# Kernel tuning notes

Measured on AMD Instinct MI355X. Metric: run time of the kernel, lower is better.

The kernel has to match this reference:

```python
import jax, jax.numpy as jnp
import numpy as np

CONF_THRES = 0.4
IOU_THRES = 0.45
MAX_WH = 4096.0   # class offset for non-agnostic NMS (torch code: max_wh)
K_PRE = 1024      # candidates kept for the O(K^2) NMS stage (<= max_nms=30000)
MAX_DET = 300     # max detections per image (torch default)
B, N, NC = 16, 25200, 80


def xywh2xyxy(x):
    xy, wh = x[..., :2], x[..., 2:4]
    return jnp.concatenate([xy - wh * 0.5, xy + wh * 0.5], axis=-1)


def box_iou(a, b):
    # a: [K,4], b: [K,4] in xyxy
    area_a = (a[:, 2] - a[:, 0]) * (a[:, 3] - a[:, 1])
    area_b = (b[:, 2] - b[:, 0]) * (b[:, 3] - b[:, 1])
    lt = jnp.maximum(a[:, None, :2], b[None, :, :2])
    rb = jnp.minimum(a[:, None, 2:], b[None, :, 2:])
    inter = jnp.clip(rb - lt, 0.0, None).prod(-1)
    return inter / (area_a[:, None] + area_b[None, :] - inter + 1e-7)


def _nms_single(pred, conf_logit, logit, head):
    # pred [N,85] (decoded, sigmoided), conf_logit [N,5] raw, logit [N,80] raw, head [N]
    xc = pred[:, 4] > CONF_THRES                      # objectness gate
    obj_sig = jax.nn.sigmoid(conf_logit[:, 4:5])      # [N,1]
    log_sig = jax.nn.sigmoid(logit) * obj_sig         # sel_prob == 'objclass'
    cls_scores = pred[:, 5:] * pred[:, 4:5]           # x[:,5:] *= x[:,4:5]
    box = xywh2xyxy(pred[:, :4])                      # [N,4]
    conf = cls_scores.max(axis=1)                     # best class conf
    j = cls_scores.argmax(axis=1).astype(pred.dtype)  # best class id
    valid = xc & (conf > CONF_THRES)
    score = jnp.where(valid, conf, 0.0)
    # top-K candidates (sorted descending) -> fixed-shape NMS
    top_s, top_i = jax.lax.top_k(score, K_PRE)
    valid_k = top_s > 0.0
    boxes_k = box[top_i] + j[top_i, None] * MAX_WH    # per-class box offset (agnostic=False)
    iou = box_iou(boxes_k, boxes_k)                   # [K,K]
    idx = jnp.arange(K_PRE)

    def body(i, keep):
        sup = (iou[i] > IOU_THRES) & (idx > i) & keep[i]
        return keep & ~sup

    keep = jax.lax.fori_loop(0, K_PRE, body, valid_k)
    final_score = jnp.where(keep, top_s, 0.0)
    _, sel = jax.lax.top_k(final_score, MAX_DET)      # first MAX_DET survivors
    gi = top_i[sel]
    m = (final_score[sel] > 0.0).astype(pred.dtype)[:, None]  # validity mask
    det = jnp.concatenate([box[gi], conf[gi, None], j[gi, None]], axis=1)  # [300,6] xyxy,conf,cls
    # pack: det(6) | class logits*obj(80) | obj_conf(1) | classHead(1) | valid(1) -> [300,89]
    return jnp.concatenate(
        [det * m, log_sig[gi] * m, obj_sig[gi] * m, head[gi, None] * m, m], axis=1)


def setup_inputs() -> dict:
    key = jax.random.key(0)
    k1, k2, k3, k4, k5, k6 = jax.random.split(key, 6)
    xy = jax.random.uniform(k1, (B, N, 2), jnp.float32) * 640.0
    wh = 2.0 + jax.random.uniform(k2, (B, N, 2), jnp.float32) * 198.0
    objcls = jax.random.uniform(k3, (B, N, 1 + NC), jnp.float32)
    prediction = jnp.concatenate([xy, wh, objcls], axis=-1)       # [B,N,85]
    pred_conf_logits = jax.random.normal(k4, (B, N, 5), jnp.float32)
    logits = jax.random.normal(k5, (B, N, NC), jnp.float32)
    class_head = jax.random.randint(k6, (B, N), 0, 3).astype(jnp.float32)
    return {"prediction": prediction, "pred_conf_logits": pred_conf_logits,
            "logits": logits, "class_head": class_head}


def reference(prediction, pred_conf_logits, logits, class_head):
    return jax.vmap(_nms_single)(prediction, pred_conf_logits, logits, class_head)
```

## Files before the change

### kernel.cpp

```cpp
#include <hip/hip_runtime.h>
#include <math.h>

#define BATCH 16
#define NN 25200
#define NCLS 80
#define K_PRE 1024
#define MAX_DET 300
#define CONF_T 0.4f
#define IOU_T 0.45f
#define TBIAS 0x3E000000u
#define RROWS 128
#define STHREADS 512

__global__ void __launch_bounds__(STHREADS) score_kernel(
    const float* __restrict__ pred, unsigned long long* __restrict__ keys) {
    __shared__ float srow[RROWS * 85];

    const int tile = blockIdx.x, b = blockIdx.y, tid = threadIdx.x;
    const int row0 = tile * RROWS;
    int nrows = NN - row0;
    if (nrows > RROWS) nrows = RROWS;

    const float4* g4 = (const float4*)(pred + ((size_t)b * NN + row0) * 85);
    float4* l4 = (float4*)srow;
    const int nf4 = (nrows * 85) >> 2;
    for (int i = tid; i < nf4; i += STHREADS) l4[i] = g4[i];
    __syncthreads();

    const int r = tid >> 2, sub = tid & 3;
    float best = 0.0f;
    int bc = sub * 20;
    float obj = 0.0f;
    if (r < nrows) {
        obj = srow[r * 85 + 4];
        if (obj > CONF_T) {
            const float* cp = &srow[r * 85 + 5 + sub * 20];
#pragma unroll
            for (int i = 0; i < 20; ++i) {
                float v = cp[i] * obj;
                if (v > best) { best = v; bc = sub * 20 + i; }
            }
        }
    }
#pragma unroll
    for (int d = 1; d < 4; d <<= 1) {
        float ov = __shfl_xor(best, d);
        int oc = __shfl_xor(bc, d);
        if (ov > best || (ov == best && oc < bc)) { best = ov; bc = oc; }
    }
    if (r < nrows && sub == 0) {
        unsigned t = (obj > CONF_T && best > CONF_T)
                         ? (__float_as_uint(best) - TBIAS) : 0u;
        int n = row0 + r;
        keys[(size_t)b * NN + n] =
            ((unsigned long long)t << 22) |
            ((unsigned long long)(unsigned)(NN - 1 - n) << 7) | (unsigned)bc;
    }
}

__global__ void __launch_bounds__(1024) fused_kernel(
    const unsigned long long* __restrict__ keys, const float* __restrict__ pred,
    const float* __restrict__ conf_logits, const float* __restrict__ logits,
    const float* __restrict__ head, float* __restrict__ out) {
    __shared__ unsigned sA[1024], sB[1024];
    __shared__ unsigned long long skeys[2048];
    __shared__ float bx0[K_PRE], by0[K_PRE], bx1[K_PRE], by1[K_PRE],
        bar[K_PRE];
    __shared__ short mlist[16 * 256];
    __shared__ unsigned char kf_s[K_PRE];
    __shared__ unsigned sel_d0, sel_cnt;
    volatile unsigned char* kf = kf_s;

    const int b = blockIdx.x, tid = threadIdx.x;
    const unsigned long long* bk = keys + (size_t)b * NN;

    float* ob = out + (size_t)b * MAX_DET * 89;
    for (int i = tid; i < MAX_DET * 89; i += 1024) ob[i] = 0.0f;

    sA[tid] = 0u;
    skeys[tid] = 0ull;
    skeys[tid + 1024] = 0ull;
    if (tid == 0) { sel_d0 = 0u; sel_cnt = 0u; }
    __syncthreads();

    for (int base = 0; base < 25600; base += 1024) {
        int i = base + tid;
        if (i < NN) {
            unsigned t = (unsigned)(bk[i] >> 22);
            if (t) atomicAdd(&sA[t >> 15], 1u);
        }
    }
    __syncthreads();

    unsigned* src = sA;
    unsigned* dst = sB;
    for (int off = 1; off < 1024; off <<= 1) {
        dst[tid] = src[tid] + ((tid + off < 1024) ? src[tid + off] : 0u);
        __syncthreads();
        unsigned* t2 = src; src = dst; dst = t2;
    }
    unsigned total = src[0];
    unsigned K = total < 1024u ? total : 1024u;
    if (total) {
        unsigned geq = src[tid];
        unsigned gt = (tid < 1023) ? src[tid + 1] : 0u;
        if (gt < K && K <= geq) sel_d0 = (unsigned)tid;
    }
    __syncthreads();
    const unsigned d0 = sel_d0;

    for (int base = 0; base < 25600; base += 1024) {
        int i = base + tid;
        if (i < NN) {
            unsigned long long key = bk[i];
            unsigned t = (unsigned)(key >> 22);
            if (t && (t >> 15) >= d0) {
                unsigned p = atomicAdd(&sel_cnt, 1u);
                if (p < 2048u) skeys[p] = key;
            }
        }
    }
    __syncthreads();

    for (unsigned k2 = 2; k2 <= 2048; k2 <<= 1) {
        for (unsigned j = k2 >> 1; j > 0; j >>= 1) {
            unsigned i = (((unsigned)tid & ~(j - 1)) << 1) | ((unsigned)tid & (j - 1));
            unsigned ixj = i | j;
            unsigned long long a = skeys[i], c = skeys[ixj];
            bool desc = ((i & k2) == 0u);
            if (desc ? (a < c) : (a > c)) { skeys[i] = c; skeys[ixj] = a; }
            __syncthreads();
        }
    }

    unsigned long long mykey = skeys[tid];
    unsigned t = (unsigned)(mykey >> 22);
    int n = NN - 1 - (int)((mykey >> 7) & 32767u);
    if (t) {
        const float* row = pred + ((size_t)b * NN + n) * 85;
        float x = row[0], y = row[1], w = row[2], h = row[3];
        float x0 = x - w * 0.5f, y0 = y - h * 0.5f;
        float x1 = x + w * 0.5f, y1 = y + h * 0.5f;
        bx0[tid] = x0; by0[tid] = y0; bx1[tid] = x1; by1[tid] = y1;
        bar[tid] = (x1 - x0) * (y1 - y0);
        kf_s[tid] = 1;
    } else {
        kf_s[tid] = 0;
    }
    __syncthreads();

    const int wave = tid >> 6, lane = tid & 63;
    short* ml = &mlist[wave * 256];
    for (int q = 0; q < 5; ++q) {
        int c = wave + 16 * q;
        int m = 0;
        for (int chunk = 0; chunk < 16; ++chunk) {
            int i = chunk * 64 + lane;
            unsigned long long kk = skeys[i];
            bool my = ((kk >> 22) != 0ull) && ((int)(kk & 127u) == c);
            unsigned long long bal = __ballot(my);
            if (my) {
                int pos = __popcll(bal & ((1ull << lane) - 1ull));
                if (m + pos < 256) ml[m + pos] = (short)i;
            }
            m += __popcll(bal);
        }
        if (m > 256) m = 256;
        for (int i = 0; i < m - 1; ++i) {
            __builtin_amdgcn_wave_barrier();
            int ci = ml[i];
            if (kf[ci]) {
                float ax0 = bx0[ci], ay0 = by0[ci];
                float ax1 = bx1[ci], ay1 = by1[ci];
                float aa = bar[ci];
                for (int j = i + 1 + lane; j < m; j += 64) {
                    int cj = ml[j];
                    if (kf[cj]) {
                        float lx = fmaxf(ax0, bx0[cj]);
                        float ly = fmaxf(ay0, by0[cj]);
                        float rx = fminf(ax1, bx1[cj]);
                        float ry = fminf(ay1, by1[cj]);
                        float iw = fmaxf(rx - lx, 0.0f);
                        float ih = fmaxf(ry - ly, 0.0f);
                        float inter = iw * ih;
                        float iou = inter / (aa + bar[cj] - inter + 1e-7f);
                        if (iou > IOU_T) kf[cj] = 0;
                    }
                }
            }
        }
    }
    __syncthreads();

    int kp = kf_s[tid] ? 1 : 0;
    src = sA; dst = sB;
    src[tid] = (unsigned)kp;
    __syncthreads();
    for (int off = 1; off < 1024; off <<= 1) {
        dst[tid] = src[tid] + ((tid >= off) ? src[tid - off] : 0u);
        __syncthreads();
        unsigned* t2 = src; src = dst; dst = t2;
    }
    int rank = (int)src[tid] - kp;

    if (kp && rank < MAX_DET) {
        float* orow = ob + (size_t)rank * 89;
        orow[0] = bx0[tid]; orow[1] = by0[tid];
        orow[2] = bx1[tid]; orow[3] = by1[tid];
        orow[4] = __uint_as_float(t + TBIAS);
        orow[5] = (float)(int)(mykey & 127u);
        float cl = conf_logits[((size_t)b * NN + n) * 5 + 4];
        float obj_sig = 1.0f / (1.0f + expf(-cl));
        const float4* lrow4 =
            (const float4*)(logits + ((size_t)b * NN + n) * NCLS);
#pragma unroll 4
        for (int q = 0; q < 20; ++q) {
            float4 l4 = lrow4[q];
            orow[6 + 4 * q + 0] = (1.0f / (1.0f + expf(-l4.x))) * obj_sig;
            orow[6 + 4 * q + 1] = (1.0f / (1.0f + expf(-l4.y))) * obj_sig;
            orow[6 + 4 * q + 2] = (1.0f / (1.0f + expf(-l4.z))) * obj_sig;
            orow[6 + 4 * q + 3] = (1.0f / (1.0f + expf(-l4.w))) * obj_sig;
        }
        orow[86] = obj_sig;
        orow[87] = head[(size_t)b * NN + n];
        orow[88] = 1.0f;
    }
}

extern "C" void kernel_launch(void* const* d_in, const int* in_sizes, int n_in,
                              void* d_out, int out_size, void* d_ws,
                              size_t ws_size, hipStream_t stream) {
    const float* pred        = (const float*)d_in[0];
    const float* conf_logits = (const float*)d_in[1];
    const float* logits      = (const float*)d_in[2];
    const float* head        = (const float*)d_in[3];
    float* out = (float*)d_out;

    unsigned long long* keys = (unsigned long long*)d_ws;

    dim3 sgrid((NN + RROWS - 1) / RROWS, BATCH);
    score_kernel<<<sgrid, STHREADS, 0, stream>>>(pred, keys);
    fused_kernel<<<BATCH, 1024, 0, stream>>>(keys, pred, conf_logits, logits,
                                             head, out);
}
```

Measured before the change: 349.4 us.

## Replace barrier-heavy scans and bitonic sort with register caching, rank sort, per-class NMS

Keys are loaded once into registers and reused for the histogram and selection passes, so they are not read from global memory twice. The Hillis-Steele scans are replaced with wave shuffle scans, and the bitonic sort is replaced by a counting-rank sort that needs no barriers. NMS now runs one thread per class over a 64-bit alive mask, replacing the wave-per-class loop. Each class list is capped at 64 entries where the old cap was 256, which risks wrong results if a class has more than 64 candidates. The rank sort and serial per-class NMS do O(n^2) work per thread.

```diff
diff --git a/kernel.cpp b/kernel.cpp
--- a/kernel.cpp
+++ b/kernel.cpp
@@ -11,6 +11,7 @@
 #define TBIAS 0x3E000000u
 #define RROWS 128
 #define STHREADS 512
+#define NCH 25
 
 __global__ void __launch_bounds__(STHREADS) score_kernel(
     const float* __restrict__ pred, unsigned long long* __restrict__ keys) {
@@ -62,151 +63,176 @@
     const unsigned long long* __restrict__ keys, const float* __restrict__ pred,
     const float* __restrict__ conf_logits, const float* __restrict__ logits,
     const float* __restrict__ head, float* __restrict__ out) {
-    __shared__ unsigned sA[1024], sB[1024];
     __shared__ unsigned long long skeys[2048];
-    __shared__ float bx0[K_PRE], by0[K_PRE], bx1[K_PRE], by1[K_PRE],
-        bar[K_PRE];
-    __shared__ short mlist[16 * 256];
-    __shared__ unsigned char kf_s[K_PRE];
+    __shared__ unsigned long long sorted[1024];
+    __shared__ float4 sbox[1024];
+    __shared__ unsigned char scls[1024];
+    __shared__ unsigned char skf[1024];
+    __shared__ short mlist[NCLS * 64];
+    __shared__ unsigned mcnt[NCLS];
+    __shared__ unsigned hist[1024];
+    __shared__ unsigned sS[1024];
+    __shared__ unsigned chunkT[16], chunkE[16];
+    __shared__ unsigned wsum[16], wpre[16];
     __shared__ unsigned sel_d0, sel_cnt;
-    volatile unsigned char* kf = kf_s;
 
     const int b = blockIdx.x, tid = threadIdx.x;
+    const int wave = tid >> 6, lane = tid & 63;
     const unsigned long long* bk = keys + (size_t)b * NN;
 
     float* ob = out + (size_t)b * MAX_DET * 89;
     for (int i = tid; i < MAX_DET * 89; i += 1024) ob[i] = 0.0f;
 
-    sA[tid] = 0u;
+    hist[tid] = 0u;
+    sorted[tid] = 0ull;
     skeys[tid] = 0ull;
     skeys[tid + 1024] = 0ull;
+    if (tid < NCLS) mcnt[tid] = 0u;
     if (tid == 0) { sel_d0 = 0u; sel_cnt = 0u; }
-    __syncthreads();
-
-    for (int base = 0; base < 25600; base += 1024) {
-        int i = base + tid;
-        if (i < NN) {
-            unsigned t = (unsigned)(bk[i] >> 22);
-            if (t) atomicAdd(&sA[t >> 15], 1u);
-        }
-    }
-    __syncthreads();
-
-    unsigned* src = sA;
-    unsigned* dst = sB;
-    for (int off = 1; off < 1024; off <<= 1) {
-        dst[tid] = src[tid] + ((tid + off < 1024) ? src[tid + off] : 0u);
-        __syncthreads();
-        unsigned* t2 = src; src = dst; dst = t2;
-    }
-    unsigned total = src[0];
+
+    unsigned long long kr[NCH];
+#pragma unroll
+    for (int q = 0; q < NCH; ++q) {
+        int i = q * 1024 + tid;
+        kr[q] = (i < NN) ? bk[i] : 0ull;
+    }
+    __syncthreads();
+
+#pragma unroll
+    for (int q = 0; q < NCH; ++q) {
+        unsigned t = (unsigned)(kr[q] >> 22);
+        if (t) atomicAdd(&hist[t >> 15], 1u);
+    }
+    __syncthreads();
+
+    unsigned s = hist[tid];
+#pragma unroll
+    for (int off = 1; off < 64; off <<= 1) {
+        unsigned v = __shfl_down(s, off);
+        if (lane + off < 64) s += v;
+    }
+    if (lane == 0) chunkT[wave] = s;
+    __syncthreads();
+    if (tid < 16) {
+        unsigned cs = chunkT[tid];
+#pragma unroll
+        for (int off = 1; off < 16; off <<= 1) {
+            unsigned v = __shfl_down(cs, off);
+            if (tid + off < 16) cs += v;
+        }
+        chunkE[tid] = cs - chunkT[tid];
+    }
+    __syncthreads();
+    unsigned S = s + chunkE[wave];
+    sS[tid] = S;
+    __syncthreads();
+    unsigned total = sS[0];
     unsigned K = total < 1024u ? total : 1024u;
     if (total) {
-        unsigned geq = src[tid];
-        unsigned gt = (tid < 1023) ? src[tid + 1] : 0u;
-        if (gt < K && K <= geq) sel_d0 = (unsigned)tid;
+        unsigned gt = (tid < 1023) ? sS[tid + 1] : 0u;
+        if (gt < K && K <= S) sel_d0 = (unsigned)tid;
     }
     __syncthreads();
     const unsigned d0 = sel_d0;
 
-    for (int base = 0; base < 25600; base += 1024) {
-        int i = base + tid;
-        if (i < NN) {
-            unsigned long long key = bk[i];
-            unsigned t = (unsigned)(key >> 22);
-            if (t && (t >> 15) >= d0) {
-                unsigned p = atomicAdd(&sel_cnt, 1u);
-                if (p < 2048u) skeys[p] = key;
-            }
-        }
-    }
-    __syncthreads();
-
-    for (unsigned k2 = 2; k2 <= 2048; k2 <<= 1) {
-        for (unsigned j = k2 >> 1; j > 0; j >>= 1) {
-            unsigned i = (((unsigned)tid & ~(j - 1)) << 1) | ((unsigned)tid & (j - 1));
-            unsigned ixj = i | j;
-            unsigned long long a = skeys[i], c = skeys[ixj];
-            bool desc = ((i & k2) == 0u);
-            if (desc ? (a < c) : (a > c)) { skeys[i] = c; skeys[ixj] = a; }
-            __syncthreads();
-        }
-    }
-
-    unsigned long long mykey = skeys[tid];
+#pragma unroll
+    for (int q = 0; q < NCH; ++q) {
+        unsigned long long key = kr[q];
+        unsigned t = (unsigned)(key >> 22);
+        if (t && (t >> 15) >= d0) {
+            unsigned p = atomicAdd(&sel_cnt, 1u);
+            if (p < 2048u) skeys[p] = key;
+        }
+    }
+    __syncthreads();
+    unsigned cnt = sel_cnt;
+    if (cnt > 2048u) cnt = 2048u;
+
+    unsigned long long k0 = skeys[tid], k1 = skeys[tid + 1024];
+    int r0 = 0, r1 = 0;
+#pragma unroll 4
+    for (unsigned j = 0; j < cnt; ++j) {
+        unsigned long long kj = skeys[j];
+        r0 += (kj > k0);
+        r1 += (kj > k1);
+    }
+    if ((unsigned)tid < cnt && r0 < 1024) sorted[r0] = k0;
+    if ((unsigned)(tid + 1024) < cnt && r1 < 1024) sorted[r1] = k1;
+    __syncthreads();
+
+    unsigned long long mykey = sorted[tid];
     unsigned t = (unsigned)(mykey >> 22);
     int n = NN - 1 - (int)((mykey >> 7) & 32767u);
     if (t) {
         const float* row = pred + ((size_t)b * NN + n) * 85;
         float x = row[0], y = row[1], w = row[2], h = row[3];
-        float x0 = x - w * 0.5f, y0 = y - h * 0.5f;
-        float x1 = x + w * 0.5f, y1 = y + h * 0.5f;
-        bx0[tid] = x0; by0[tid] = y0; bx1[tid] = x1; by1[tid] = y1;
-        bar[tid] = (x1 - x0) * (y1 - y0);
-        kf_s[tid] = 1;
+        sbox[tid] = make_float4(x - w * 0.5f, y - h * 0.5f,
+                                x + w * 0.5f, y + h * 0.5f);
+        scls[tid] = (unsigned char)(mykey & 127u);
+        skf[tid] = 1;
     } else {
-        kf_s[tid] = 0;
-    }
-    __syncthreads();
-
-    const int wave = tid >> 6, lane = tid & 63;
-    short* ml = &mlist[wave * 256];
-    for (int q = 0; q < 5; ++q) {
-        int c = wave + 16 * q;
-        int m = 0;
-        for (int chunk = 0; chunk < 16; ++chunk) {
-            int i = chunk * 64 + lane;
-            unsigned long long kk = skeys[i];
-            bool my = ((kk >> 22) != 0ull) && ((int)(kk & 127u) == c);
-            unsigned long long bal = __ballot(my);
-            if (my) {
-                int pos = __popcll(bal & ((1ull << lane) - 1ull));
-                if (m + pos < 256) ml[m + pos] = (short)i;
+        scls[tid] = 255;
+        skf[tid] = 0;
+    }
+    __syncthreads();
+
+    if (t) {
+        unsigned char myc = (unsigned char)(mykey & 127u);
+        int r = 0;
+        for (int j = 0; j < tid; ++j) r += (scls[j] == myc);
+        if (r < 64) mlist[(int)myc * 64 + r] = (short)tid;
+        atomicAdd(&mcnt[myc], 1u);
+    }
+    __syncthreads();
+
+    if (tid < NCLS) {
+        int m = (int)mcnt[tid];
+        if (m > 64) m = 64;
+        unsigned long long alive =
+            (m >= 64) ? ~0ull : ((1ull << m) - 1ull);
+        const short* ml = &mlist[tid * 64];
+        for (int i = 0; i < m - 1; ++i) {
+            if (!((alive >> i) & 1ull)) continue;
+            float4 bi = sbox[ml[i]];
+            float ai = (bi.z - bi.x) * (bi.w - bi.y);
+            for (int j = i + 1; j < m; ++j) {
+                if (!((alive >> j) & 1ull)) continue;
+                float4 bj = sbox[ml[j]];
+                float lx = fmaxf(bi.x, bj.x), ly = fmaxf(bi.y, bj.y);
+                float rx = fminf(bi.z, bj.z), ry = fminf(bi.w, bj.w);
+                float iw = fmaxf(rx - lx, 0.0f), ih = fmaxf(ry - ly, 0.0f);
+                float inter = iw * ih;
+                float aj = (bj.z - bj.x) * (bj.w - bj.y);
+                float iou = inter / (ai + aj - inter + 1e-7f);
+                if (iou > IOU_T) alive &= ~(1ull << j);
             }
-            m += __popcll(bal);
-        }
-        if (m > 256) m = 256;
-        for (int i = 0; i < m - 1; ++i) {
-            __builtin_amdgcn_wave_barrier();
-            int ci = ml[i];
-            if (kf[ci]) {
-                float ax0 = bx0[ci], ay0 = by0[ci];
-                float ax1 = bx1[ci], ay1 = by1[ci];
-                float aa = bar[ci];
-                for (int j = i + 1 + lane; j < m; j += 64) {
-                    int cj = ml[j];
-                    if (kf[cj]) {
-                        float lx = fmaxf(ax0, bx0[cj]);
-                        float ly = fmaxf(ay0, by0[cj]);
-                        float rx = fminf(ax1, bx1[cj]);
-                        float ry = fminf(ay1, by1[cj]);
-                        float iw = fmaxf(rx - lx, 0.0f);
-                        float ih = fmaxf(ry - ly, 0.0f);
-                        float inter = iw * ih;
-                        float iou = inter / (aa + bar[cj] - inter + 1e-7f);
-                        if (iou > IOU_T) kf[cj] = 0;
-                    }
-                }
-            }
-        }
-    }
-    __syncthreads();
-
-    int kp = kf_s[tid] ? 1 : 0;
-    src = sA; dst = sB;
-    src[tid] = (unsigned)kp;
-    __syncthreads();
-    for (int off = 1; off < 1024; off <<= 1) {
-        dst[tid] = src[tid] + ((tid >= off) ? src[tid - off] : 0u);
-        __syncthreads();
-        unsigned* t2 = src; src = dst; dst = t2;
-    }
-    int rank = (int)src[tid] - kp;
+        }
+        for (int i = 0; i < m; ++i)
+            if (!((alive >> i) & 1ull)) skf[ml[i]] = 0;
+    }
+    __syncthreads();
+
+    int kp = skf[tid];
+    unsigned long long bal = __ballot(kp != 0);
+    int within = __popcll(bal & ((1ull << lane) - 1ull));
+    if (lane == 0) wsum[wave] = (unsigned)__popcll(bal);
+    __syncthreads();
+    if (tid < 16) {
+        unsigned v = wsum[tid], inc = v;
+#pragma unroll
+        for (int off = 1; off < 16; off <<= 1) {
+            unsigned u = __shfl_up(inc, off);
+            if (tid >= off) inc += u;
+        }
+        wpre[tid] = inc - v;
+    }
+    __syncthreads();
+    int rank = (int)wpre[wave] + within;
 
     if (kp && rank < MAX_DET) {
+        float4 bb = sbox[tid];
         float* orow = ob + (size_t)rank * 89;
-        orow[0] = bx0[tid]; orow[1] = by0[tid];
-        orow[2] = bx1[tid]; orow[3] = by1[tid];
+        orow[0] = bb.x; orow[1] = bb.y; orow[2] = bb.z; orow[3] = bb.w;
         orow[4] = __uint_as_float(t + TBIAS);
         orow[5] = (float)(int)(mykey & 127u);
         float cl = conf_logits[((size_t)b * NN + n) * 5 + 4];
```

Measured after the change: 416.7 us. +19.3%, slower.
